# Performance work log

Measured on AMD Instinct MI355X. Metric: run time of the kernel, lower is better.

## Reference

```python
import jax, jax.numpy as jnp
import numpy as np

N_NODES = 50000
N_EDGES = 800000
IN, HID, OUT = 96, 96, 64


def setup_inputs() -> dict:
    key = jax.random.key(0)
    ks = jax.random.split(key, 12)
    x = jax.random.normal(ks[0], (N_NODES, IN), dtype=jnp.float32)
    src = jax.random.randint(ks[1], (N_EDGES,), 0, N_NODES, dtype=jnp.int32)
    dst = jax.random.randint(ks[2], (N_EDGES,), 0, N_NODES, dtype=jnp.int32)
    dims = [(IN, HID), (HID, HID), (HID, OUT)]
    params = {}
    for i, (din, dout) in enumerate(dims):
        s = 1.0 / np.sqrt(din)
        params[f"w_self{i}"] = jax.random.uniform(ks[3 + 3 * i], (dout, din), jnp.float32, -s, s)
        params[f"w_neigh{i}"] = jax.random.uniform(ks[4 + 3 * i], (dout, din), jnp.float32, -s, s)
        params[f"b{i}"] = jnp.zeros((dout,), jnp.float32)
    return {"x": x, "src": src, "dst": dst, **params}


def _sage_layer(h, src, dst, w_self, w_neigh, b):
    # mean aggregation of source-node features onto destination nodes
    msum = jax.ops.segment_sum(h[src], dst, num_segments=N_NODES)  # [N, d]
    deg = jax.ops.segment_sum(jnp.ones((src.shape[0],), h.dtype), dst, num_segments=N_NODES)
    hmean = msum / jnp.maximum(deg, 1.0)[:, None]
    return h @ w_self.T + hmean @ w_neigh.T + b


def reference(x, src, dst,
              w_self0, w_neigh0, b0,
              w_self1, w_neigh1, b1,
              w_self2, w_neigh2, b2):
    # Layer 0 + ReLU (dropout is identity in eval mode)
    h = jax.nn.relu(_sage_layer(x, src, dst, w_self0, w_neigh0, b0))
    # Layer 1 + ReLU
    h = jax.nn.relu(_sage_layer(h, src, dst, w_self1, w_neigh1, b1))
    # Final layer, no activation
    h = _sage_layer(h, src, dst, w_self2, w_neigh2, b2)
    return h
```

## Files before the change

kernel.cpp:

```cpp
#include <hip/hip_runtime.h>
#include <hip/hip_fp16.h>


#define DIN 96

typedef __attribute__((ext_vector_type(8))) _Float16 f16x8;
typedef __attribute__((ext_vector_type(16))) float f32x16;

__global__ void zero_deg_kernel(int* __restrict__ p, int n) {
    int i = blockIdx.x * blockDim.x + threadIdx.x;
    if (i < n) p[i] = 0;
}

__global__ void deg_kernel(const int* __restrict__ dst, int* __restrict__ deg,
                           int* __restrict__ rank, int nE) {
    int i = blockIdx.x * blockDim.x + threadIdx.x;
    if (i < nE) rank[i] = atomicAdd(&deg[dst[i]], 1);
}

__global__ void block_sum_kernel(const int* __restrict__ deg, int* __restrict__ bsum, int nN) {
    __shared__ int s[256];
    const int tid = threadIdx.x;
    int i = blockIdx.x * 256 + tid;
    s[tid] = (i < nN) ? deg[i] : 0;
    __syncthreads();
    for (int d = 128; d > 0; d >>= 1) {
        if (tid < d) s[tid] += s[tid + d];
        __syncthreads();
    }
    if (tid == 0) bsum[blockIdx.x] = s[0];
}

__global__ void bsum_scan_kernel(int* __restrict__ bsum, int nB) {
    __shared__ int s[256];
    const int tid = threadIdx.x;
    int v = (tid < nB) ? bsum[tid] : 0;
    s[tid] = v;
    __syncthreads();
    for (int d = 1; d < 256; d <<= 1) {
        int t = (tid >= d) ? s[tid - d] : 0;
        __syncthreads();
        s[tid] += t;
        __syncthreads();
    }
    if (tid < nB) bsum[tid] = s[tid] - v;
}

__global__ void scan_apply_kernel(const int* __restrict__ deg, const int* __restrict__ bsum,
                                  int* __restrict__ offs, int nN) {
    __shared__ int s[256];
    const int tid = threadIdx.x;
    int i = blockIdx.x * 256 + tid;
    int v = (i < nN) ? deg[i] : 0;
    s[tid] = v;
    __syncthreads();
    for (int d = 1; d < 256; d <<= 1) {
        int t = (tid >= d) ? s[tid - d] : 0;
        __syncthreads();
        s[tid] += t;
        __syncthreads();
    }
    if (i < nN) offs[i] = bsum[blockIdx.x] + s[tid] - v;
}

__global__ void bucket_kernel(const int* __restrict__ src, const int* __restrict__ dst,
                              const int* __restrict__ offs, const int* __restrict__ rank,
                              unsigned short* __restrict__ esrc, int nE) {
    int e = blockIdx.x * blockDim.x + threadIdx.x;
    if (e < nE) esrc[offs[dst[e]] + rank[e]] = (unsigned short)src[e];
}

__global__ void tof16_kernel(const float* __restrict__ x, __half* __restrict__ xf, int n8) {
    int i = blockIdx.x * blockDim.x + threadIdx.x;
    if (i >= n8) return;
    float4 f0 = *reinterpret_cast<const float4*>(x + (size_t)i * 8);
    float4 f1 = *reinterpret_cast<const float4*>(x + (size_t)i * 8 + 4);
    union { __half2 h2[4]; float4 raw; } o;
    o.h2[0] = __float22half2_rn(make_float2(f0.x, f0.y));
    o.h2[1] = __float22half2_rn(make_float2(f0.z, f0.w));
    o.h2[2] = __float22half2_rn(make_float2(f1.x, f1.y));
    o.h2[3] = __float22half2_rn(make_float2(f1.z, f1.w));
    *reinterpret_cast<float4*>(xf + (size_t)i * 8) = o.raw;
}

__global__ void gather_kernel(const __half* __restrict__ hf, const unsigned short* __restrict__ esrc,
                              const int* __restrict__ offs, const int* __restrict__ deg,
                              __half* __restrict__ hmean, int nN) {
    int idx = blockIdx.x * blockDim.x + threadIdx.x;
    if (idx >= nN * 12) return;
    int n = idx / 12;
    int q = idx - n * 12;
    const int beg = offs[n];
    const int dg = deg[n];
    const int end = beg + dg;
    const __half* hq = hf + q * 8;

    union H8 { float4 raw; __half2 h2[4]; };
    float a0[8], a1[8], a2[8], a3[8];
#pragma unroll
    for (int k = 0; k < 8; ++k) { a0[k] = 0.f; a1[k] = 0.f; a2[k] = 0.f; a3[k] = 0.f; }

    int j = beg;
    for (; j + 4 <= end; j += 4) {
        int s0 = esrc[j], s1 = esrc[j + 1], s2 = esrc[j + 2], s3 = esrc[j + 3];
        H8 v0, v1, v2, v3;
        v0.raw = *reinterpret_cast<const float4*>(hq + (size_t)s0 * DIN);
        v1.raw = *reinterpret_cast<const float4*>(hq + (size_t)s1 * DIN);
        v2.raw = *reinterpret_cast<const float4*>(hq + (size_t)s2 * DIN);
        v3.raw = *reinterpret_cast<const float4*>(hq + (size_t)s3 * DIN);
#pragma unroll
        for (int k = 0; k < 4; ++k) {
            float2 f0 = __half22float2(v0.h2[k]);
            float2 f1 = __half22float2(v1.h2[k]);
            float2 f2 = __half22float2(v2.h2[k]);
            float2 f3 = __half22float2(v3.h2[k]);
            a0[2 * k] += f0.x; a0[2 * k + 1] += f0.y;
            a1[2 * k] += f1.x; a1[2 * k + 1] += f1.y;
            a2[2 * k] += f2.x; a2[2 * k + 1] += f2.y;
            a3[2 * k] += f3.x; a3[2 * k + 1] += f3.y;
        }
    }
    for (; j < end; ++j) {
        int s0 = esrc[j];
        H8 v0;
        v0.raw = *reinterpret_cast<const float4*>(hq + (size_t)s0 * DIN);
#pragma unroll
        for (int k = 0; k < 4; ++k) {
            float2 f0 = __half22float2(v0.h2[k]);
            a0[2 * k] += f0.x; a0[2 * k + 1] += f0.y;
        }
    }
    const float r = 1.0f / (float)max(dg, 1);
    union H8 o;
    o.h2[0] = __float22half2_rn(make_float2((a0[0]+a1[0]+a2[0]+a3[0])*r, (a0[1]+a1[1]+a2[1]+a3[1])*r));
    o.h2[1] = __float22half2_rn(make_float2((a0[2]+a1[2]+a2[2]+a3[2])*r, (a0[3]+a1[3]+a2[3]+a3[3])*r));
    o.h2[2] = __float22half2_rn(make_float2((a0[4]+a1[4]+a2[4]+a3[4])*r, (a0[5]+a1[5]+a2[5]+a3[5])*r));
    o.h2[3] = __float22half2_rn(make_float2((a0[6]+a1[6]+a2[6]+a3[6])*r, (a0[7]+a1[7]+a2[7]+a3[7])*r));
    *reinterpret_cast<float4*>(hmean + (size_t)n * DIN + q * 8) = o.raw;
}

template<int DOUT, int NP, bool RELU, bool FINAL>
__global__ __launch_bounds__(256)
void sage_gemm_mfma(const __half* __restrict__ hp, const __half* __restrict__ hm,
                    const float* __restrict__ wself, const float* __restrict__ wneigh,
                    const float* __restrict__ bias, float* __restrict__ fout,
                    __half* __restrict__ hout, int nN) {
    __shared__ unsigned int WS[DOUT][100];

    const int tid = threadIdx.x;
    const int n0 = blockIdx.x * 256;

    for (int c = tid; c < DOUT * 24; c += 256) {
        int r = c / 24, k8 = c - (c / 24) * 24;
        const float* srcw = (k8 < 12) ? (wself + (size_t)r * 96 + k8 * 8)
                                      : (wneigh + (size_t)r * 96 + (k8 - 12) * 8);
        float4 f0 = *reinterpret_cast<const float4*>(srcw);
        float4 f1 = *reinterpret_cast<const float4*>(srcw + 4);
        union { __half2 h2[4]; unsigned int u[4]; } o;
        o.h2[0] = __float22half2_rn(make_float2(f0.x, f0.y));
        o.h2[1] = __float22half2_rn(make_float2(f0.z, f0.w));
        o.h2[2] = __float22half2_rn(make_float2(f1.x, f1.y));
        o.h2[3] = __float22half2_rn(make_float2(f1.z, f1.w));
        WS[r][k8 * 4 + 0] = o.u[0];
        WS[r][k8 * 4 + 1] = o.u[1];
        WS[r][k8 * 4 + 2] = o.u[2];
        WS[r][k8 * 4 + 3] = o.u[3];
    }
    __syncthreads();

    const int lane = tid & 63;
    const int w = tid >> 6;
    const int col = lane & 31;
    const int q = lane >> 5;
    const int mbase = n0 + w * 64;

    const int nA0 = min(mbase + col, nN - 1);
    const int nA1 = min(mbase + 32 + col, nN - 1);

    f32x16 acc[NP][2];
#pragma unroll
    for (int p = 0; p < NP; ++p) {
        f32x16 z = {};
        acc[p][0] = z;
        acc[p][1] = z;
    }

#pragma unroll
    for (int ks = 0; ks < 12; ++ks) {
        const __half* s0 = (ks < 6) ? (hp + (size_t)nA0 * 96 + ks * 16 + q * 8)
                                    : (hm + (size_t)nA0 * 96 + (ks - 6) * 16 + q * 8);
        const __half* s1 = (ks < 6) ? (hp + (size_t)nA1 * 96 + ks * 16 + q * 8)
                                    : (hm + (size_t)nA1 * 96 + (ks - 6) * 16 + q * 8);
        union { float4 raw; f16x8 v; } a0, a1;
        a0.raw = *reinterpret_cast<const float4*>(s0);
        a1.raw = *reinterpret_cast<const float4*>(s1);

#pragma unroll
        for (int p = 0; p < NP; ++p) {
            const f16x8 wv = *reinterpret_cast<const f16x8*>(&WS[p * 32 + col][ks * 8 + q * 4]);
            acc[p][0] = __builtin_amdgcn_mfma_f32_32x32x16_f16(a0.v, wv, acc[p][0], 0, 0, 0);
            acc[p][1] = __builtin_amdgcn_mfma_f32_32x32x16_f16(a1.v, wv, acc[p][1], 0, 0, 0);
        }
    }

#pragma unroll
    for (int p = 0; p < NP; ++p) {
        const int oc = p * 32 + col;
        const float bv = bias[oc];
#pragma unroll
        for (int i = 0; i < 16; ++i) {
            const int row = (i & 3) + 8 * (i >> 2) + 4 * q;
            int n = mbase + row;
            if (n < nN) {
                float v = acc[p][0][i] + bv;
                if (RELU) v = fmaxf(v, 0.f);
                if (FINAL) fout[(size_t)n * DOUT + oc] = v;
                else       hout[(size_t)n * DOUT + oc] = __float2half_rn(v);
            }
            n = mbase + 32 + row;
            if (n < nN) {
                float v = acc[p][1][i] + bv;
                if (RELU) v = fmaxf(v, 0.f);
                if (FINAL) fout[(size_t)n * DOUT + oc] = v;
                else       hout[(size_t)n * DOUT + oc] = __float2half_rn(v);
            }
        }
    }
}

extern "C" void kernel_launch(void* const* d_in, const int* in_sizes, int n_in,
                              void* d_out, int out_size, void* d_ws, size_t ws_size,
                              hipStream_t stream) {
    const float* x   = (const float*)d_in[0];
    const int*   src = (const int*)d_in[1];
    const int*   dst = (const int*)d_in[2];
    const float* ws0 = (const float*)d_in[3];
    const float* wn0 = (const float*)d_in[4];
    const float* b0  = (const float*)d_in[5];
    const float* ws1 = (const float*)d_in[6];
    const float* wn1 = (const float*)d_in[7];
    const float* b1  = (const float*)d_in[8];
    const float* ws2 = (const float*)d_in[9];
    const float* wn2 = (const float*)d_in[10];
    const float* b2  = (const float*)d_in[11];
    float* out = (float*)d_out;

    const int nN = in_sizes[0] / DIN;
    const int nE = in_sizes[1];
    const int nB = (nN + 255) / 256;

    int* deg  = (int*)d_ws;
    int* offs = deg + 50048;
    int* bsum = offs + 50048;
    int* rank = bsum + 256;
    unsigned short* esrc = (unsigned short*)(rank + nE);
    __half* hp16 = (__half*)(esrc + nE);
    __half* hm16 = hp16 + (size_t)nN * DIN;

    zero_deg_kernel<<<nB, 256, 0, stream>>>(deg, nN);
    deg_kernel<<<(nE + 255) / 256, 256, 0, stream>>>(dst, deg, rank, nE);
    block_sum_kernel<<<nB, 256, 0, stream>>>(deg, bsum, nN);
    bsum_scan_kernel<<<1, 256, 0, stream>>>(bsum, nB);
    scan_apply_kernel<<<nB, 256, 0, stream>>>(deg, bsum, offs, nN);
    bucket_kernel<<<(nE + 255) / 256, 256, 0, stream>>>(src, dst, offs, rank, esrc, nE);

    const int cgrid = (nN * 12 + 255) / 256;
    const int ggrid = (nN * 12 + 255) / 256;
    const int mgrid = (nN + 255) / 256;

    tof16_kernel<<<cgrid, 256, 0, stream>>>(x, hp16, nN * 12);
    gather_kernel<<<ggrid, 256, 0, stream>>>(hp16, esrc, offs, deg, hm16, nN);
    sage_gemm_mfma<96, 3, true, false><<<mgrid, 256, 0, stream>>>(hp16, hm16, ws0, wn0, b0, nullptr, hp16, nN);

    gather_kernel<<<ggrid, 256, 0, stream>>>(hp16, esrc, offs, deg, hm16, nN);
    sage_gemm_mfma<96, 3, true, false><<<mgrid, 256, 0, stream>>>(hp16, hm16, ws1, wn1, b1, nullptr, hp16, nN);

    gather_kernel<<<ggrid, 256, 0, stream>>>(hp16, esrc, offs, deg, hm16, nN);
    sage_gemm_mfma<64, 2, false, true><<<mgrid, 256, 0, stream>>>(hp16, hm16, ws2, wn2, b2, out, nullptr, nN);
}
```

Baseline: 212.3 us.

## Sort nodes by degree bucket to balance gather work within wavefronts

Adds a degree histogram (capped at 63), scans it, and builds a permutation of nodes grouped by degree. The gather kernel then assigns threads to nodes through this permutation, so threads in a wavefront handle nodes with similar edge counts and divergence in the per-node loop is reduced. The cost is extra atomics in the scan kernels, a perm array lookup, and scattered writes to hmean and reads of offs/deg, which can hurt coalescing and locality.

```diff
diff --git a/kernel.cpp b/kernel.cpp
--- a/kernel.cpp
+++ b/kernel.cpp
@@ -18,20 +18,27 @@
     if (i < nE) rank[i] = atomicAdd(&deg[dst[i]], 1);
 }
 
-__global__ void block_sum_kernel(const int* __restrict__ deg, int* __restrict__ bsum, int nN) {
+__global__ void block_sum_kernel(const int* __restrict__ deg, int* __restrict__ bsum,
+                                 int* __restrict__ bins, int nN) {
     __shared__ int s[256];
+    __shared__ int lbins[64];
     const int tid = threadIdx.x;
+    if (tid < 64) lbins[tid] = 0;
     int i = blockIdx.x * 256 + tid;
-    s[tid] = (i < nN) ? deg[i] : 0;
-    __syncthreads();
+    int v = (i < nN) ? deg[i] : 0;
+    s[tid] = v;
+    __syncthreads();
+    if (i < nN) atomicAdd(&lbins[min(v, 63)], 1);
     for (int d = 128; d > 0; d >>= 1) {
         if (tid < d) s[tid] += s[tid + d];
         __syncthreads();
     }
     if (tid == 0) bsum[blockIdx.x] = s[0];
-}
-
-__global__ void bsum_scan_kernel(int* __restrict__ bsum, int nB) {
+    if (tid < 64 && lbins[tid]) atomicAdd(&bins[tid], lbins[tid]);
+}
+
+__global__ void bsum_scan_kernel(int* __restrict__ bsum, int nB,
+                                 const int* __restrict__ bins, int* __restrict__ binCur) {
     __shared__ int s[256];
     const int tid = threadIdx.x;
     int v = (tid < nB) ? bsum[tid] : 0;
@@ -44,10 +51,22 @@
         __syncthreads();
     }
     if (tid < nB) bsum[tid] = s[tid] - v;
+    __syncthreads();
+    int bv = (tid < 64) ? bins[tid] : 0;
+    s[tid] = bv;
+    __syncthreads();
+    for (int d = 1; d < 64; d <<= 1) {
+        int t = (tid >= d && tid < 64) ? s[tid - d] : 0;
+        __syncthreads();
+        if (tid < 64) s[tid] += t;
+        __syncthreads();
+    }
+    if (tid < 64) binCur[tid] = s[tid] - bv;
 }
 
 __global__ void scan_apply_kernel(const int* __restrict__ deg, const int* __restrict__ bsum,
-                                  int* __restrict__ offs, int nN) {
+                                  int* __restrict__ offs, int* __restrict__ binCur,
+                                  int* __restrict__ perm, int nN) {
     __shared__ int s[256];
     const int tid = threadIdx.x;
     int i = blockIdx.x * 256 + tid;
@@ -60,7 +79,11 @@
         s[tid] += t;
         __syncthreads();
     }
-    if (i < nN) offs[i] = bsum[blockIdx.x] + s[tid] - v;
+    if (i < nN) {
+        offs[i] = bsum[blockIdx.x] + s[tid] - v;
+        int pos = atomicAdd(&binCur[min(v, 63)], 1);
+        perm[pos] = i;
+    }
 }
 
 __global__ void bucket_kernel(const int* __restrict__ src, const int* __restrict__ dst,
@@ -85,11 +108,12 @@
 
 __global__ void gather_kernel(const __half* __restrict__ hf, const unsigned short* __restrict__ esrc,
                               const int* __restrict__ offs, const int* __restrict__ deg,
+                              const int* __restrict__ perm,
                               __half* __restrict__ hmean, int nN) {
     int idx = blockIdx.x * blockDim.x + threadIdx.x;
     if (idx >= nN * 12) return;
-    int n = idx / 12;
-    int q = idx - n * 12;
+    int n = perm[idx / 12];
+    int q = idx - (idx / 12) * 12;
     const int beg = offs[n];
     const int dg = deg[n];
     const int end = beg + dg;
@@ -249,19 +273,22 @@
     const int nE = in_sizes[1];
     const int nB = (nN + 255) / 256;
 
-    int* deg  = (int*)d_ws;
-    int* offs = deg + 50048;
-    int* bsum = offs + 50048;
-    int* rank = bsum + 256;
-    unsigned short* esrc = (unsigned short*)(rank + nE);
+    int* deg    = (int*)d_ws;
+    int* bins   = deg + 50048;
+    int* binCur = bins + 64;
+    int* offs   = binCur + 64;
+    int* bsum   = offs + 50048;
+    int* rank   = bsum + 256;
+    int* perm   = rank + nE;
+    unsigned short* esrc = (unsigned short*)(perm + 50048);
     __half* hp16 = (__half*)(esrc + nE);
     __half* hm16 = hp16 + (size_t)nN * DIN;
 
-    zero_deg_kernel<<<nB, 256, 0, stream>>>(deg, nN);
+    zero_deg_kernel<<<(nN + 64 + 255) / 256, 256, 0, stream>>>(deg, nN + 64 + 64);
     deg_kernel<<<(nE + 255) / 256, 256, 0, stream>>>(dst, deg, rank, nE);
-    block_sum_kernel<<<nB, 256, 0, stream>>>(deg, bsum, nN);
-    bsum_scan_kernel<<<1, 256, 0, stream>>>(bsum, nB);
-    scan_apply_kernel<<<nB, 256, 0, stream>>>(deg, bsum, offs, nN);
+    block_sum_kernel<<<nB, 256, 0, stream>>>(deg, bsum, bins, nN);
+    bsum_scan_kernel<<<1, 256, 0, stream>>>(bsum, nB, bins, binCur);
+    scan_apply_kernel<<<nB, 256, 0, stream>>>(deg, bsum, offs, binCur, perm, nN);
     bucket_kernel<<<(nE + 255) / 256, 256, 0, stream>>>(src, dst, offs, rank, esrc, nE);
 
     const int cgrid = (nN * 12 + 255) / 256;
@@ -269,12 +296,12 @@
     const int mgrid = (nN + 255) / 256;
 
     tof16_kernel<<<cgrid, 256, 0, stream>>>(x, hp16, nN * 12);
-    gather_kernel<<<ggrid, 256, 0, stream>>>(hp16, esrc, offs, deg, hm16, nN);
+    gather_kernel<<<ggrid, 256, 0, stream>>>(hp16, esrc, offs, deg, perm, hm16, nN);
     sage_gemm_mfma<96, 3, true, false><<<mgrid, 256, 0, stream>>>(hp16, hm16, ws0, wn0, b0, nullptr, hp16, nN);
 
-    gather_kernel<<<ggrid, 256, 0, stream>>>(hp16, esrc, offs, deg, hm16, nN);
+    gather_kernel<<<ggrid, 256, 0, stream>>>(hp16, esrc, offs, deg, perm, hm16, nN);
     sage_gemm_mfma<96, 3, true, false><<<mgrid, 256, 0, stream>>>(hp16, hm16, ws1, wn1, b1, nullptr, hp16, nN);
 
-    gather_kernel<<<ggrid, 256, 0, stream>>>(hp16, esrc, offs, deg, hm16, nN);
+    gather_kernel<<<ggrid, 256, 0, stream>>>(hp16, esrc, offs, deg, perm, hm16, nN);
     sage_gemm_mfma<64, 2, false, true><<<mgrid, 256, 0, stream>>>(hp16, hm16, ws2, wn2, b2, out, nullptr, nN);
 }
```

New measurement: 340.5 us. 1.6x slower.
